# Optimization experiments

Hardware: AMD Instinct MI355X
Metric: run time of the kernel (lower is better)

Reference implementation:

```python
import jax, jax.numpy as jnp
import numpy as np

N, F_NODE, F_EDGE = 1024, 64, 32
F_IN = 2 * F_NODE + F_EDGE  # 160


def setup_inputs() -> dict:
    key = jax.random.key(0)
    ks = jax.random.split(key, 6)
    H = jax.random.normal(ks[0], (N, F_NODE), dtype=jnp.float32)
    A = jax.random.randint(ks[1], (N, N), 0, 2).astype(jnp.float32)
    E = jax.random.normal(ks[2], (N, N, F_EDGE), dtype=jnp.float32)
    # params: reset_parameters_uniform -> U(-s, s), s = 1/sqrt(dim0)
    s = 1.0 / np.sqrt(F_IN)
    W = jax.random.uniform(ks[3], (F_IN, F_NODE), jnp.float32, -s, s)
    W_att = jax.random.uniform(ks[4], (F_IN, F_NODE), jnp.float32, -s, s)
    sb = 1.0 / np.sqrt(F_NODE)
    bias = jax.random.uniform(ks[5], (F_NODE,), jnp.float32, -sb, sb)
    return {"H": H, "A": A, "E": E, "W": W, "W_att": W_att, "bias": bias}


def reference(H, A, E, W, W_att, bias):
    n = H.shape[0]
    # all-pairs concat: HE[a,b] = [H[a], H[b], E[a,b]]  -> [N, N, 2F+Fe]
    H_row = jnp.broadcast_to(H[:, None, :], (n, n, H.shape[1]))  # H2: repeat over dim 1
    H_col = jnp.broadcast_to(H[None, :, :], (n, n, H.shape[1]))  # H1: repeat over dim 0
    HE = jnp.concatenate([H_row, H_col, E], axis=2) * A[:, :, None]
    Hp = jnp.einsum('abi,ij->abj', HE, W) + bias
    Ha = jnp.einsum('abi,ij->abj', HE, W_att) + bias
    gated = jax.nn.relu(Hp) * jax.nn.sigmoid(Ha)
    return jnp.sum(gated, axis=1)
```

## Files before the change

kernel.cpp:

```cpp
#include <hip/hip_runtime.h>

#define NN 1024
#define FN 64
#define FE 32
#define FIN 160

typedef __bf16 bf16x8 __attribute__((ext_vector_type(8)));
typedef short  short8 __attribute__((ext_vector_type(8)));
typedef float  f32x4  __attribute__((ext_vector_type(4)));

static __device__ __forceinline__ unsigned short f2b(float x){
    unsigned int u = __float_as_uint(x);
    unsigned int r = (u + 0x7fffu + ((u >> 16) & 1u)) >> 16;
    return (unsigned short)r;
}

static __device__ __forceinline__ float fast_sigmoid(float y){
    return __builtin_amdgcn_rcpf(1.0f + __expf(-y));
}

static __device__ __forceinline__ bf16x8 ldfrag(const unsigned short* p){
    return __builtin_bit_cast(bf16x8, *(const short8*)p);
}

__global__ void prep(const float* __restrict__ H, const float* __restrict__ W,
                     const float* __restrict__ Wa,
                     unsigned short* __restrict__ Hb,
                     unsigned short* __restrict__ WtE,
                     unsigned short* __restrict__ WtA){
    int bid = blockIdx.x, tid = threadIdx.x;
    if (bid < 64){
        int i = (bid*256 + tid)*4;
        float4 v = *(const float4*)(H + i);
        ushort4 o;
        o.x = f2b(v.x); o.y = f2b(v.y); o.z = f2b(v.z); o.w = f2b(v.w);
        *(ushort4*)(Hb + i) = o;
    } else {
        const float* src = (bid == 64) ? W : Wa;
        unsigned short* dst = (bid == 64) ? WtE : WtA;
        for (int idx = tid; idx < FIN*FN; idx += 256){
            int k = idx >> 6, j = idx & 63;
            dst[j*FIN + k] = f2b(src[idx]);
        }
    }
}

__global__ __launch_bounds__(256) void mga_main(
    const float* __restrict__ A, const float* __restrict__ E,
    const unsigned short* __restrict__ Hb,
    const unsigned short* __restrict__ WtE, const unsigned short* __restrict__ WtA,
    const float* __restrict__ bias, float* __restrict__ out)
{
    int a    = blockIdx.x;
    int tid  = threadIdx.x;
    int wave = tid >> 6, lane = tid & 63;
    int col  = lane & 15, quad = lane >> 4;
    int half = wave >> 1, mh = wave & 1;

    __shared__ float arow[NN];
    __shared__ float red[16*FN];

    ((float4*)arow)[tid] = ((const float4*)(A + (size_t)a*NN))[tid];

    bf16x8 Bw[2][3], Ba[2][3];
    #pragma unroll
    for (int tl = 0; tl < 2; tl++){
        int n = (2*half + tl)*16 + col;
        #pragma unroll
        for (int s = 0; s < 3; s++){
            Bw[tl][s] = ldfrag(WtE + n*FIN + (s+2)*32 + quad*8);
            Ba[tl][s] = ldfrag(WtA + n*FIN + (s+2)*32 + quad*8);
        }
    }

    bf16x8 ha0 = ldfrag(Hb + a*FN + quad*8);
    bf16x8 ha1 = ldfrag(Hb + a*FN + 32 + quad*8);
    const f32x4 zero = {0.f, 0.f, 0.f, 0.f};
    f32x4 cw[2], ca[2];
    float g0[2], acc[2];
    #pragma unroll
    for (int tl = 0; tl < 2; tl++){
        int n = (2*half + tl)*16 + col;
        float bj = bias[n];
        f32x4 cb = {bj, bj, bj, bj};
        bf16x8 b0 = ldfrag(WtE + n*FIN + quad*8);
        bf16x8 b1 = ldfrag(WtE + n*FIN + 32 + quad*8);
        cw[tl] = __builtin_amdgcn_mfma_f32_16x16x32_bf16(ha1, b1,
                 __builtin_amdgcn_mfma_f32_16x16x32_bf16(ha0, b0, cb, 0,0,0), 0,0,0);
        b0 = ldfrag(WtA + n*FIN + quad*8);
        b1 = ldfrag(WtA + n*FIN + 32 + quad*8);
        ca[tl] = __builtin_amdgcn_mfma_f32_16x16x32_bf16(ha1, b1,
                 __builtin_amdgcn_mfma_f32_16x16x32_bf16(ha0, b0, cb, 0,0,0), 0,0,0);
        g0[tl] = fmaxf(bj, 0.f) * fast_sigmoid(bj);
        acc[tl] = 0.f;
    }

    __syncthreads();

    for (int c = 0; c < 16; c++){
        int b0r = c*64;

        bf16x8 ef[2], hb0[2], hb1[2];
        #pragma unroll
        for (int mt = 0; mt < 2; mt++){
            int brow = b0r + mh*32 + mt*16 + col;
            const float* ep = E + ((size_t)a*NN + brow)*FE + quad*8;
            float4 e0 = *(const float4*)(ep);
            float4 e1 = *(const float4*)(ep + 4);
            short8 afs;
            afs[0]=(short)f2b(e0.x); afs[1]=(short)f2b(e0.y);
            afs[2]=(short)f2b(e0.z); afs[3]=(short)f2b(e0.w);
            afs[4]=(short)f2b(e1.x); afs[5]=(short)f2b(e1.y);
            afs[6]=(short)f2b(e1.z); afs[7]=(short)f2b(e1.w);
            ef[mt]  = __builtin_bit_cast(bf16x8, afs);
            hb0[mt] = ldfrag(Hb + brow*FN + quad*8);
            hb1[mt] = ldfrag(Hb + brow*FN + 32 + quad*8);
        }

        #pragma unroll
        for (int mt = 0; mt < 2; mt++){
            float4 av = *(const float4*)(arow + b0r + mh*32 + mt*16 + quad*4);
            #pragma unroll
            for (int tl = 0; tl < 2; tl++){
                f32x4 pw = __builtin_amdgcn_mfma_f32_16x16x32_bf16(ef[mt], Bw[tl][2],
                           __builtin_amdgcn_mfma_f32_16x16x32_bf16(hb1[mt], Bw[tl][1],
                           __builtin_amdgcn_mfma_f32_16x16x32_bf16(hb0[mt], Bw[tl][0],
                               cw[tl], 0,0,0), 0,0,0), 0,0,0);
                f32x4 pa = __builtin_amdgcn_mfma_f32_16x16x32_bf16(ef[mt], Ba[tl][2],
                           __builtin_amdgcn_mfma_f32_16x16x32_bf16(hb1[mt], Ba[tl][1],
                           __builtin_amdgcn_mfma_f32_16x16x32_bf16(hb0[mt], Ba[tl][0],
                               ca[tl], 0,0,0), 0,0,0), 0,0,0);
                float* avp = (float*)&av;
                #pragma unroll
                for (int r = 0; r < 4; r++){
                    float f = fmaxf(pw[r], 0.f) * fast_sigmoid(pa[r]);
                    acc[tl] += (avp[r] != 0.f) ? f : g0[tl];
                }
            }
        }
    }

    #pragma unroll
    for (int tl = 0; tl < 2; tl++)
        red[(wave*4 + quad)*FN + (2*half + tl)*16 + col] = acc[tl];
    __syncthreads();
    if (tid < FN){
        int base = (tid >= 32) ? 8 : 0;
        float s = 0.f;
        #pragma unroll
        for (int r = 0; r < 8; r++) s += red[(base + r)*FN + tid];
        out[a*FN + tid] = s;
    }
}

extern "C" void kernel_launch(void* const* d_in, const int* in_sizes, int n_in,
                              void* d_out, int out_size, void* d_ws, size_t ws_size,
                              hipStream_t stream) {
    const float* H    = (const float*)d_in[0];
    const float* A    = (const float*)d_in[1];
    const float* E    = (const float*)d_in[2];
    const float* W    = (const float*)d_in[3];
    const float* Wa   = (const float*)d_in[4];
    const float* bias = (const float*)d_in[5];
    float* out = (float*)d_out;

    unsigned short* Hb  = (unsigned short*)d_ws;
    unsigned short* WtE = Hb + NN*FN;
    unsigned short* WtA = WtE + FN*FIN;

    prep    <<<dim3(66),   dim3(256), 0, stream>>>(H, W, Wa, Hb, WtE, WtA);
    mga_main<<<dim3(NN),   dim3(256), 0, stream>>>(A, E, Hb, WtE, WtA, bias, out);
}
```

Before: 270.2 us.

## Split neighbor dimension across 4 blocks per row with partial-sum reduce kernel

Each output row is now computed by 4 blocks, each covering a quarter of the b range, and the partial sums are written to workspace and combined by a new reduction kernel. This raises the grid from 1024 to 4096 blocks to improve load balance and latency hiding across CUs, at the cost of repeated per-block weight/prologue loads, an extra launch, and a partial buffer round-trip. E-to-bf16 conversion also switches from round-to-nearest to truncation via a byte-permute, cutting ALU work per element but slightly changing numerics.

Result: faster. 260.1 us (-3.8%).

```diff
diff --git a/kernel.cpp b/kernel.cpp
--- a/kernel.cpp
+++ b/kernel.cpp
@@ -4,6 +4,7 @@
 #define FN 64
 #define FE 32
 #define FIN 160
+#define NS 4
 
 typedef __bf16 bf16x8 __attribute__((ext_vector_type(8)));
 typedef short  short8 __attribute__((ext_vector_type(8)));
@@ -20,7 +21,11 @@
 }
 
 static __device__ __forceinline__ bf16x8 ldfrag(const unsigned short* p){
-    return __builtin_bit_cast(bf16x8, *(const short8*)p);
+    return __builtin_bit_cast(bf16x8, *(const short8*)(p));
+}
+
+static __device__ __forceinline__ unsigned packtrunc(float lo, float hi){
+    return __builtin_amdgcn_perm(__float_as_uint(hi), __float_as_uint(lo), 0x07060302u);
 }
 
 __global__ void prep(const float* __restrict__ H, const float* __restrict__ W,
@@ -49,33 +54,34 @@
     const float* __restrict__ A, const float* __restrict__ E,
     const unsigned short* __restrict__ Hb,
     const unsigned short* __restrict__ WtE, const unsigned short* __restrict__ WtA,
-    const float* __restrict__ bias, float* __restrict__ out)
+    const float* __restrict__ bias, float* __restrict__ part)
 {
-    int a    = blockIdx.x;
+    int bid  = blockIdx.x;
+    int a    = bid / NS, s = bid % NS;
     int tid  = threadIdx.x;
     int wave = tid >> 6, lane = tid & 63;
     int col  = lane & 15, quad = lane >> 4;
     int half = wave >> 1, mh = wave & 1;
+    int bbase = s * (NN / NS);
 
-    __shared__ float arow[NN];
+    __shared__ float arow[NN/NS];
     __shared__ float red[16*FN];
 
-    ((float4*)arow)[tid] = ((const float4*)(A + (size_t)a*NN))[tid];
+    arow[tid] = A[(size_t)a*NN + bbase + tid];
 
     bf16x8 Bw[2][3], Ba[2][3];
     #pragma unroll
     for (int tl = 0; tl < 2; tl++){
         int n = (2*half + tl)*16 + col;
         #pragma unroll
-        for (int s = 0; s < 3; s++){
-            Bw[tl][s] = ldfrag(WtE + n*FIN + (s+2)*32 + quad*8);
-            Ba[tl][s] = ldfrag(WtA + n*FIN + (s+2)*32 + quad*8);
+        for (int sg = 0; sg < 3; sg++){
+            Bw[tl][sg] = ldfrag(WtE + n*FIN + (sg+2)*32 + quad*8);
+            Ba[tl][sg] = ldfrag(WtA + n*FIN + (sg+2)*32 + quad*8);
         }
     }
 
     bf16x8 ha0 = ldfrag(Hb + a*FN + quad*8);
     bf16x8 ha1 = ldfrag(Hb + a*FN + 32 + quad*8);
-    const f32x4 zero = {0.f, 0.f, 0.f, 0.f};
     f32x4 cw[2], ca[2];
     float g0[2], acc[2];
     #pragma unroll
@@ -97,22 +103,22 @@
 
     __syncthreads();
 
-    for (int c = 0; c < 16; c++){
-        int b0r = c*64;
+    for (int cc = 0; cc < NN/NS/64; cc++){
+        int b0r = cc*64;
 
         bf16x8 ef[2], hb0[2], hb1[2];
         #pragma unroll
         for (int mt = 0; mt < 2; mt++){
-            int brow = b0r + mh*32 + mt*16 + col;
+            int brow = bbase + b0r + mh*32 + mt*16 + col;
             const float* ep = E + ((size_t)a*NN + brow)*FE + quad*8;
             float4 e0 = *(const float4*)(ep);
             float4 e1 = *(const float4*)(ep + 4);
-            short8 afs;
-            afs[0]=(short)f2b(e0.x); afs[1]=(short)f2b(e0.y);
-            afs[2]=(short)f2b(e0.z); afs[3]=(short)f2b(e0.w);
-            afs[4]=(short)f2b(e1.x); afs[5]=(short)f2b(e1.y);
-            afs[6]=(short)f2b(e1.z); afs[7]=(short)f2b(e1.w);
-            ef[mt]  = __builtin_bit_cast(bf16x8, afs);
+            int4 pk;
+            pk.x = (int)packtrunc(e0.x, e0.y);
+            pk.y = (int)packtrunc(e0.z, e0.w);
+            pk.z = (int)packtrunc(e1.x, e1.y);
+            pk.w = (int)packtrunc(e1.z, e1.w);
+            ef[mt]  = __builtin_bit_cast(bf16x8, pk);
             hb0[mt] = ldfrag(Hb + brow*FN + quad*8);
             hb1[mt] = ldfrag(Hb + brow*FN + 32 + quad*8);
         }
@@ -146,11 +152,22 @@
     __syncthreads();
     if (tid < FN){
         int base = (tid >= 32) ? 8 : 0;
-        float s = 0.f;
+        float sum = 0.f;
         #pragma unroll
-        for (int r = 0; r < 8; r++) s += red[(base + r)*FN + tid];
-        out[a*FN + tid] = s;
+        for (int r = 0; r < 8; r++) sum += red[(base + r)*FN + tid];
+        part[((size_t)s*NN + a)*FN + tid] = sum;
     }
+}
+
+__global__ void mga_reduce(const float* __restrict__ part, float* __restrict__ out){
+    int i = blockIdx.x*256 + threadIdx.x;
+    float4 v = ((const float4*)part)[i];
+    #pragma unroll
+    for (int s = 1; s < NS; s++){
+        float4 p = ((const float4*)(part + (size_t)s*NN*FN))[i];
+        v.x += p.x; v.y += p.y; v.z += p.z; v.w += p.w;
+    }
+    ((float4*)out)[i] = v;
 }
 
 extern "C" void kernel_launch(void* const* d_in, const int* in_sizes, int n_in,
@@ -167,7 +184,9 @@
     unsigned short* Hb  = (unsigned short*)d_ws;
     unsigned short* WtE = Hb + NN*FN;
     unsigned short* WtA = WtE + FN*FIN;
+    float* part = (float*)(WtA + FN*FIN);
 
-    prep    <<<dim3(66),   dim3(256), 0, stream>>>(H, W, Wa, Hb, WtE, WtA);
-    mga_main<<<dim3(NN),   dim3(256), 0, stream>>>(A, E, Hb, WtE, WtA, bias, out);
+    prep      <<<dim3(66),      dim3(256), 0, stream>>>(H, W, Wa, Hb, WtE, WtA);
+    mga_main  <<<dim3(NN*NS),   dim3(256), 0, stream>>>(A, E, Hb, WtE, WtA, bias, part);
+    mga_reduce<<<dim3(64),      dim3(256), 0, stream>>>(part, out);
 }
```
